# Performance work log

Measured on AMD Instinct MI355X. Metric: run time of the kernel, lower is better.

The kernel has to match this reference:

```python
import jax, jax.numpy as jnp
import numpy as np

N_NODES = 100000
N_EDGES = 1600000
D_IN = 64
D_HID = 64
D_ACT = 16


def gcn_conv(x, W, b, src, dst, n_nodes):
    """PyG-style GCNConv: D^-1/2 (A+I) D^-1/2 (x @ W) + b."""
    h = x @ W  # [N, out]
    ones = jnp.ones(src.shape[0], dtype=x.dtype)
    # degree with self-loops (in-degree + 1)
    deg = jax.ops.segment_sum(ones, dst, num_segments=n_nodes) + 1.0
    dinv = jax.lax.rsqrt(deg)  # [N]
    coef = dinv[src] * dinv[dst]  # [E]
    agg = jax.ops.segment_sum(h[src] * coef[:, None], dst, num_segments=n_nodes)
    agg = agg + h * (dinv * dinv)[:, None]  # self-loop term
    return agg + b


def setup_inputs() -> dict:
    key = jax.random.key(0)
    ks = jax.random.split(key, 6)
    x = jax.random.normal(ks[0], (N_NODES, D_IN), dtype=jnp.float32)
    edge_index = jax.random.randint(ks[1], (2, N_EDGES), 0, N_NODES, dtype=jnp.int64)
    s1 = 1.0 / np.sqrt(D_IN)
    s2 = 1.0 / np.sqrt(D_HID)
    W1 = jax.random.normal(ks[2], (D_IN, D_HID), dtype=jnp.float32) * s1
    b1 = jnp.zeros((D_HID,), dtype=jnp.float32)
    W2 = jax.random.normal(ks[3], (D_HID, D_HID), dtype=jnp.float32) * s2
    b2 = jnp.zeros((D_HID,), dtype=jnp.float32)
    Wfc = jax.random.normal(ks[4], (D_HID, D_ACT), dtype=jnp.float32) * s2
    bfc = jnp.zeros((D_ACT,), dtype=jnp.float32)
    return {"x": x, "edge_index": edge_index, "W1": W1, "b1": b1,
            "W2": W2, "b2": b2, "Wfc": Wfc, "bfc": bfc}


def reference(x, edge_index, W1, b1, W2, b2, Wfc, bfc):
    src, dst = edge_index[0], edge_index[1]
    n = x.shape[0]
    h = jax.nn.relu(gcn_conv(x, W1, b1, src, dst, n))
    h = jax.nn.relu(gcn_conv(h, W2, b2, src, dst, n))
    q_values = h @ Wfc + bfc
    return q_values
```

## Files before the change

### kernel.cpp

```cpp
#include <hip/hip_runtime.h>

#define NN 100000
#define NE 1600000
#define NCAP 64
#define NB2 782
#define NBP2 1024
#define CAP2 2560
#define CHUNK 2048
#define NCHUNK 782

typedef __attribute__((ext_vector_type(8))) short short8;
typedef __attribute__((ext_vector_type(4))) float f32x4;

static __device__ __forceinline__ unsigned short f2bf(float f) {
    unsigned u = __float_as_uint(f);
    u += 0x7fffu + ((u >> 16) & 1u);
    return (unsigned short)(u >> 16);
}
static __device__ __forceinline__ float bflo(unsigned u) { return __uint_as_float(u << 16); }
static __device__ __forceinline__ float bfhi(unsigned u) { return __uint_as_float(u & 0xffff0000u); }

static __device__ __forceinline__ short8 as_s8(uint4 u) {
    union { uint4 u4; short8 s8; } x; x.u4 = u; return x.s8;
}
static __device__ __forceinline__ f32x4 mfma16(short8 a, short8 b, f32x4 c) {
    return __builtin_amdgcn_mfma_f32_16x16x32_bf16(a, b, c, 0, 0, 0);
}

static __device__ __forceinline__ void split8(float4 a, float4 b, short8& hi8, short8& lo8) {
    float vv[8] = {a.x, a.y, a.z, a.w, b.x, b.y, b.z, b.w};
    unsigned h[8], l[8];
    #pragma unroll
    for (int j = 0; j < 8; ++j) {
        h[j] = f2bf(vv[j]);
        l[j] = f2bf(vv[j] - bflo(h[j]));
    }
    uint4 uh, ul;
    uh.x = h[0] | (h[1] << 16); uh.y = h[2] | (h[3] << 16);
    uh.z = h[4] | (h[5] << 16); uh.w = h[6] | (h[7] << 16);
    ul.x = l[0] | (l[1] << 16); ul.y = l[2] | (l[3] << 16);
    ul.z = l[4] | (l[5] << 16); ul.w = l[6] | (l[7] << 16);
    hi8 = as_s8(uh); lo8 = as_s8(ul);
}

__global__ __launch_bounds__(256) void bin_edges(const int* __restrict__ src,
                                                 const int* __restrict__ dst,
                                                 int* __restrict__ gcur,
                                                 int* __restrict__ pairs) {
    __shared__ int lcnt[NBP2];
    __shared__ int lnext[NBP2];
    int t = threadIdx.x;
    #pragma unroll
    for (int i = 0; i < 4; ++i) lcnt[t + 256 * i] = 0;
    __syncthreads();
    int base = blockIdx.x * CHUNK;
    int sr[8], dr[8];
    #pragma unroll
    for (int i = 0; i < 8; ++i) {
        int e = base + t + 256 * i;
        bool v = e < NE;
        sr[i] = v ? src[e] : 0;
        dr[i] = v ? dst[e] : -1;
        if (v) atomicAdd(&lcnt[dr[i] >> 7], 1);
    }
    __syncthreads();
    #pragma unroll
    for (int i = 0; i < 4; ++i) {
        int b = t + 256 * i;
        int v = lcnt[b];
        if (v) lnext[b] = b * CAP2 + atomicAdd(&gcur[b], v);
    }
    __syncthreads();
    #pragma unroll
    for (int i = 0; i < 8; ++i) {
        if (dr[i] >= 0) {
            int p = atomicAdd(&lnext[dr[i] >> 7], 1);
            pairs[p] = sr[i] | ((dr[i] & 127) << 17);
        }
    }
}

__global__ __launch_bounds__(256) void slab_place(const int* __restrict__ pairs,
                                                  const int* __restrict__ gcur,
                                                  int* __restrict__ esrc,
                                                  int* __restrict__ cnt,
                                                  float* __restrict__ dinv) {
    __shared__ int lc[128];
    int b = blockIdx.x;
    int t = threadIdx.x;
    if (t < 128) lc[t] = 0;
    __syncthreads();
    int e0 = b * CAP2;
    int e1 = e0 + min(gcur[b], CAP2);
    for (int i = e0 + t; i < e1; i += 256) {
        int w = pairs[i];
        int li = w >> 17;
        int p = atomicAdd(&lc[li], 1);
        if (p < NCAP - 1) esrc[(((b << 7) + li) << 6) + p] = w & 0x1FFFF;
    }
    __syncthreads();
    if (t < 128) {
        int node = (b << 7) + t;
        if (node < NN) {
            int c = lc[t];
            int cc = min(c, NCAP - 1);
            esrc[(node << 6) + cc] = node;
            cnt[node] = cc + 1;
            dinv[node] = rsqrtf((float)c + 1.0f);
        }
    }
}

__global__ void wpack(const float* __restrict__ W1, const float* __restrict__ W2,
                      uint4* __restrict__ P, int* __restrict__ gcur) {
    int tid = blockIdx.x * blockDim.x + threadIdx.x;
    if (tid >= 1024) return;
    gcur[tid] = 0;
    int w = tid >> 9;
    int f = tid & 511;
    int c = f >> 7;
    int t = (f >> 6) & 1;
    int lane = f & 63;
    const float* W = w ? W2 : W1;
    int k0 = t * 32 + (lane >> 4) * 8;
    int n  = c * 16 + (lane & 15);
    unsigned sh[8], sl[8];
    #pragma unroll
    for (int j = 0; j < 8; ++j) {
        float v = W[(k0 + j) * 64 + n];
        sh[j] = f2bf(v);
        sl[j] = f2bf(v - bflo(sh[j]));
    }
    uint4 ph, pl;
    ph.x = sh[0] | (sh[1] << 16); ph.y = sh[2] | (sh[3] << 16);
    ph.z = sh[4] | (sh[5] << 16); ph.w = sh[6] | (sh[7] << 16);
    pl.x = sl[0] | (sl[1] << 16); pl.y = sl[2] | (sl[3] << 16);
    pl.z = sl[4] | (sl[5] << 16); pl.w = sl[6] | (sl[7] << 16);
    P[w * 1024 + f]       = ph;
    P[w * 1024 + 512 + f] = pl;
}

__global__ __launch_bounds__(256) void gemm1_mfma(const float* __restrict__ X,
                                                  const uint4* __restrict__ WP,
                                                  const float* __restrict__ dinv,
                                                  uint4* __restrict__ G4) {
    __shared__ __align__(16) unsigned short Ls[4][16][64];
    int wave = threadIdx.x >> 6, lane = threadIdx.x & 63;
    int tile = blockIdx.x * 4 + wave;
    bool active = tile < (NN / 16);
    int node0 = (active ? tile : 0) * 16;
    int r = lane & 15, g = lane >> 4;

    const float* xr = X + (size_t)(node0 + r) * 64 + g * 8;
    float4 x0a = *(const float4*)(xr);
    float4 x0b = *(const float4*)(xr + 4);
    float4 x1a = *(const float4*)(xr + 32);
    float4 x1b = *(const float4*)(xr + 36);
    short8 ah0, al0, ah1, al1;
    split8(x0a, x0b, ah0, al0);
    split8(x1a, x1b, ah1, al1);

    f32x4 acc[4];
    #pragma unroll
    for (int c = 0; c < 4; ++c) acc[c] = (f32x4){0.f, 0.f, 0.f, 0.f};
    #pragma unroll
    for (int c = 0; c < 4; ++c) {
        short8 bh0 = as_s8(WP[(c * 2 + 0) * 64 + lane]);
        short8 bl0 = as_s8(WP[512 + (c * 2 + 0) * 64 + lane]);
        short8 bh1 = as_s8(WP[(c * 2 + 1) * 64 + lane]);
        short8 bl1 = as_s8(WP[512 + (c * 2 + 1) * 64 + lane]);
        acc[c] = mfma16(ah0, bh0, acc[c]);
        acc[c] = mfma16(al0, bh0, acc[c]);
        acc[c] = mfma16(ah0, bl0, acc[c]);
        acc[c] = mfma16(ah1, bh1, acc[c]);
        acc[c] = mfma16(al1, bh1, acc[c]);
        acc[c] = mfma16(ah1, bl1, acc[c]);
    }
    float dd[4];
    #pragma unroll
    for (int rr = 0; rr < 4; ++rr) dd[rr] = dinv[node0 + g * 4 + rr];
    #pragma unroll
    for (int c = 0; c < 4; ++c) {
        #pragma unroll
        for (int rr = 0; rr < 4; ++rr)
            Ls[wave][g * 4 + rr][c * 16 + r] = f2bf(acc[c][rr] * dd[rr]);
    }
    __syncthreads();
    if (active) {
        #pragma unroll
        for (int i = 0; i < 2; ++i) {
            int idx = lane + i * 64;
            int row = idx >> 3, u = idx & 7;
            G4[(size_t)(node0 + row) * 8 + u] = *(const uint4*)&Ls[wave][row][u * 8];
        }
    }
}

__global__ __launch_bounds__(256) void gemm2_mfma(const uint4* __restrict__ X4,
                                                  const uint4* __restrict__ WP,
                                                  const float* __restrict__ dinv,
                                                  uint4* __restrict__ G4) {
    __shared__ __align__(16) unsigned short Ls[4][16][64];
    int wave = threadIdx.x >> 6, lane = threadIdx.x & 63;
    int tile = blockIdx.x * 4 + wave;
    bool active = tile < (NN / 16);
    int node0 = (active ? tile : 0) * 16;
    int r = lane & 15, g = lane >> 4;

    short8 a0 = as_s8(X4[(size_t)(node0 + r) * 8 + g]);
    short8 a1 = as_s8(X4[(size_t)(node0 + r) * 8 + 4 + g]);

    f32x4 acc[4];
    #pragma unroll
    for (int c = 0; c < 4; ++c) acc[c] = (f32x4){0.f, 0.f, 0.f, 0.f};
    #pragma unroll
    for (int c = 0; c < 4; ++c) {
        short8 bh0 = as_s8(WP[(c * 2 + 0) * 64 + lane]);
        short8 bl0 = as_s8(WP[512 + (c * 2 + 0) * 64 + lane]);
        short8 bh1 = as_s8(WP[(c * 2 + 1) * 64 + lane]);
        short8 bl1 = as_s8(WP[512 + (c * 2 + 1) * 64 + lane]);
        acc[c] = mfma16(a0, bh0, acc[c]);
        acc[c] = mfma16(a0, bl0, acc[c]);
        acc[c] = mfma16(a1, bh1, acc[c]);
        acc[c] = mfma16(a1, bl1, acc[c]);
    }
    float dd[4];
    #pragma unroll
    for (int rr = 0; rr < 4; ++rr) dd[rr] = dinv[node0 + g * 4 + rr];
    #pragma unroll
    for (int c = 0; c < 4; ++c) {
        #pragma unroll
        for (int rr = 0; rr < 4; ++rr)
            Ls[wave][g * 4 + rr][c * 16 + r] = f2bf(acc[c][rr] * dd[rr]);
    }
    __syncthreads();
    if (active) {
        #pragma unroll
        for (int i = 0; i < 2; ++i) {
            int idx = lane + i * 64;
            int row = idx >> 3, u = idx & 7;
            G4[(size_t)(node0 + row) * 8 + u] = *(const uint4*)&Ls[wave][row][u * 8];
        }
    }
}

#define ACC8(u) do { \
    a0 += bflo((u).x); a1 += bfhi((u).x); a2 += bflo((u).y); a3 += bfhi((u).y); \
    a4 += bflo((u).z); a5 += bfhi((u).z); a6 += bflo((u).w); a7 += bfhi((u).w); } while (0)

#define GATHER_CORE(node)                                                     \
    int deg = cnt[node];                                                      \
    int sidx = esrc[((node) << 6) + (lane & 31)];                             \
    int nt = (deg - e + 7) >> 3;        \
    int s0 = __shfl(sidx, e);                                                 \
    int s1 = __shfl(sidx, e + 8);                                             \
    int s2 = __shfl(sidx, e + 16);                                            \
    int s3 = __shfl(sidx, e + 24);                                            \
    float a0 = 0.f, a1 = 0.f, a2 = 0.f, a3 = 0.f,                             \
          a4 = 0.f, a5 = 0.f, a6 = 0.f, a7 = 0.f;                             \
    uint4 u0, u1, u2, u3;                                                     \
    if (nt > 0) u0 = G4[s0 * 8 + m];                                          \
    if (nt > 1) u1 = G4[s1 * 8 + m];                                          \
    if (nt > 2) u2 = G4[s2 * 8 + m];                                          \
    if (nt > 3) u3 = G4[s3 * 8 + m];                                          \
    if (nt > 0) ACC8(u0);                                                     \
    if (nt > 1) ACC8(u1);                                                     \
    if (nt > 2) ACC8(u2);                                                     \
    if (nt > 3) ACC8(u3);                                                     \
    if (__any(nt > 4)) {                          \
        int shi = esrc[((node) << 6) + 32 + (lane & 31)];                     \
        int s4 = __shfl(shi, e);                                              \
        int s5 = __shfl(shi, e + 8);                                          \
        int s6 = __shfl(shi, e + 16);                                         \
        int s7 = __shfl(shi, e + 24);                                         \
        uint4 u4, u5, u6, u7;                                                 \
        if (nt > 4) u4 = G4[s4 * 8 + m];                                      \
        if (nt > 5) u5 = G4[s5 * 8 + m];                                      \
        if (nt > 6) u6 = G4[s6 * 8 + m];                                      \
        if (nt > 7) u7 = G4[s7 * 8 + m];                                      \
        if (nt > 4) ACC8(u4);                                                 \
        if (nt > 5) ACC8(u5);                                                 \
        if (nt > 6) ACC8(u6);                                                 \
        if (nt > 7) ACC8(u7);                                                 \
    }                                                                         \
    a0 += __shfl_xor(a0, 8);  a1 += __shfl_xor(a1, 8);                        \
    a2 += __shfl_xor(a2, 8);  a3 += __shfl_xor(a3, 8);                        \
    a4 += __shfl_xor(a4, 8);  a5 += __shfl_xor(a5, 8);                        \
    a6 += __shfl_xor(a6, 8);  a7 += __shfl_xor(a7, 8);                        \
    a0 += __shfl_xor(a0, 16); a1 += __shfl_xor(a1, 16);                       \
    a2 += __shfl_xor(a2, 16); a3 += __shfl_xor(a3, 16);                       \
    a4 += __shfl_xor(a4, 16); a5 += __shfl_xor(a5, 16);                       \
    a6 += __shfl_xor(a6, 16); a7 += __shfl_xor(a7, 16);                       \
    a0 += __shfl_xor(a0, 32); a1 += __shfl_xor(a1, 32);                       \
    a2 += __shfl_xor(a2, 32); a3 += __shfl_xor(a3, 32);                       \
    a4 += __shfl_xor(a4, 32); a5 += __shfl_xor(a5, 32);                       \
    a6 += __shfl_xor(a6, 32); a7 += __shfl_xor(a7, 32);

__global__ __launch_bounds__(256) void gather_bf16(
        const int* __restrict__ cnt, const int* __restrict__ esrc,
        const float* __restrict__ dinv, const uint4* __restrict__ G4,
        const float* __restrict__ b, uint4* __restrict__ outH) {
    int node = blockIdx.x * 4 + (threadIdx.x >> 6);
    int lane = threadIdx.x & 63;
    int e = lane >> 3, m = lane & 7;
    GATHER_CORE(node)
    if (e == 0) {
        float dd = dinv[node];
        float4 b0 = ((const float4*)b)[2 * m];
        float4 b1v = ((const float4*)b)[2 * m + 1];
        float h0 = fmaxf(fmaf(a0, dd, b0.x), 0.f);
        float h1 = fmaxf(fmaf(a1, dd, b0.y), 0.f);
        float h2 = fmaxf(fmaf(a2, dd, b0.z), 0.f);
        float h3 = fmaxf(fmaf(a3, dd, b0.w), 0.f);
        float h4 = fmaxf(fmaf(a4, dd, b1v.x), 0.f);
        float h5 = fmaxf(fmaf(a5, dd, b1v.y), 0.f);
        float h6 = fmaxf(fmaf(a6, dd, b1v.z), 0.f);
        float h7 = fmaxf(fmaf(a7, dd, b1v.w), 0.f);
        uint4 pk;
        pk.x = (unsigned)f2bf(h0) | ((unsigned)f2bf(h1) << 16);
        pk.y = (unsigned)f2bf(h2) | ((unsigned)f2bf(h3) << 16);
        pk.z = (unsigned)f2bf(h4) | ((unsigned)f2bf(h5) << 16);
        pk.w = (unsigned)f2bf(h6) | ((unsigned)f2bf(h7) << 16);
        outH[(size_t)node * 8 + m] = pk;
    }
}

__global__ __launch_bounds__(256) void gather_fc(
        const int* __restrict__ cnt, const int* __restrict__ esrc,
        const float* __restrict__ dinv, const uint4* __restrict__ G4,
        const float* __restrict__ b2, const float* __restrict__ Wfc,
        const float* __restrict__ bfc, float* __restrict__ out) {
    int node = blockIdx.x * 4 + (threadIdx.x >> 6);
    int lane = threadIdx.x & 63;
    int e = lane >> 3, m = lane & 7;
    int q = lane >> 4, c = lane & 15;
    float Wreg[16];
    #pragma unroll
    for (int i = 0; i < 16; ++i) Wreg[i] = Wfc[(q * 16 + i) * 16 + c];
    GATHER_CORE(node)
    float dd = dinv[node];
    float4 b0 = ((const float4*)b2)[2 * m];
    float4 b1v = ((const float4*)b2)[2 * m + 1];
    a0 = fmaxf(fmaf(a0, dd, b0.x), 0.f);
    a1 = fmaxf(fmaf(a1, dd, b0.y), 0.f);
    a2 = fmaxf(fmaf(a2, dd, b0.z), 0.f);
    a3 = fmaxf(fmaf(a3, dd, b0.w), 0.f);
    a4 = fmaxf(fmaf(a4, dd, b1v.x), 0.f);
    a5 = fmaxf(fmaf(a5, dd, b1v.y), 0.f);
    a6 = fmaxf(fmaf(a6, dd, b1v.z), 0.f);
    a7 = fmaxf(fmaf(a7, dd, b1v.w), 0.f);
    int sl0 = 2 * q, sl1 = 2 * q + 1;
    float acc = 0.f;
    acc = fmaf(__shfl(a0, sl0), Wreg[0], acc);
    acc = fmaf(__shfl(a1, sl0), Wreg[1], acc);
    acc = fmaf(__shfl(a2, sl0), Wreg[2], acc);
    acc = fmaf(__shfl(a3, sl0), Wreg[3], acc);
    acc = fmaf(__shfl(a4, sl0), Wreg[4], acc);
    acc = fmaf(__shfl(a5, sl0), Wreg[5], acc);
    acc = fmaf(__shfl(a6, sl0), Wreg[6], acc);
    acc = fmaf(__shfl(a7, sl0), Wreg[7], acc);
    acc = fmaf(__shfl(a0, sl1), Wreg[8], acc);
    acc = fmaf(__shfl(a1, sl1), Wreg[9], acc);
    acc = fmaf(__shfl(a2, sl1), Wreg[10], acc);
    acc = fmaf(__shfl(a3, sl1), Wreg[11], acc);
    acc = fmaf(__shfl(a4, sl1), Wreg[12], acc);
    acc = fmaf(__shfl(a5, sl1), Wreg[13], acc);
    acc = fmaf(__shfl(a6, sl1), Wreg[14], acc);
    acc = fmaf(__shfl(a7, sl1), Wreg[15], acc);
    acc += __shfl_xor(acc, 16);
    acc += __shfl_xor(acc, 32);
    if (lane < 16) out[node * 16 + c] = acc + bfc[c];
}

extern "C" void kernel_launch(void* const* d_in, const int* in_sizes, int n_in,
                              void* d_out, int out_size, void* d_ws, size_t ws_size,
                              hipStream_t stream) {
    const float* x   = (const float*)d_in[0];
    const int*   ei  = (const int*)d_in[1];
    const float* W1  = (const float*)d_in[2];
    const float* b1  = (const float*)d_in[3];
    const float* W2  = (const float*)d_in[4];
    const float* b2  = (const float*)d_in[5];
    const float* Wfc = (const float*)d_in[6];
    const float* bfc = (const float*)d_in[7];
    float* out = (float*)d_out;

    const int* src = ei;
    const int* dst = ei + NE;

    int*      gcur  = (int*)d_ws;
    int*      cnt   = gcur + NBP2;
    float*    dinvp = (float*)(cnt + NN);
    int*      esrc  = (int*)(dinvp + NN);
    unsigned* G     = (unsigned*)(esrc + (size_t)NN * NCAP);
    uint4*    bufB  = (uint4*)(G + (size_t)NN * 32);
    uint4*    WPK   = (uint4*)((unsigned*)bufB + (size_t)NN * 32);
    int*      pairs = (int*)bufB;

    wpack<<<4, 256, 0, stream>>>(W1, W2, WPK, gcur);
    bin_edges<<<NCHUNK, 256, 0, stream>>>(src, dst, gcur, pairs);
    slab_place<<<NB2, 256, 0, stream>>>(pairs, gcur, esrc, cnt, dinvp);

    gemm1_mfma<<<(NN / 16 + 3) / 4, 256, 0, stream>>>(x, WPK, dinvp, (uint4*)G);
    gather_bf16<<<NN / 4, 256, 0, stream>>>(cnt, esrc, dinvp, (const uint4*)G, b1, bufB);

    gemm2_mfma<<<(NN / 16 + 3) / 4, 256, 0, stream>>>(bufB, WPK + 1024, dinvp, (uint4*)G);
    gather_fc<<<NN / 4, 256, 0, stream>>>(cnt, esrc, dinvp, (const uint4*)G, b2, Wfc, bfc, out);
}
```

Baseline: 239.7 us.

## Shard edge-bin counters into eight groups and loop gather over edge slots

Edge binning now spreads each destination bin's global atomic counter and pair region across eight sub-slabs, chosen by block index. This reduces contention on the global atomicAdd, and slab_place walks all eight sub-slabs per bin. The gather core drops the fixed shuffle-based unrolled 8-edge scheme and uses a strided loop, two edges per iteration, that reads source indices directly from esrc. Per-group capacity is 384, so a skewed group could overflow and silently drop edges. The looped gather may also expose less memory-level parallelism than the old fully unrolled loads.

Measured after the change: 228.5 us. -4.6%, faster.

```diff
diff --git a/kernel.cpp b/kernel.cpp
--- a/kernel.cpp
+++ b/kernel.cpp
@@ -5,7 +5,7 @@
 #define NCAP 64
 #define NB2 782
 #define NBP2 1024
-#define CAP2 2560
+#define CAPG 384
 #define CHUNK 2048
 #define NCHUNK 782
 
@@ -50,6 +50,7 @@
     __shared__ int lcnt[NBP2];
     __shared__ int lnext[NBP2];
     int t = threadIdx.x;
+    int grp = blockIdx.x & 7;
     #pragma unroll
     for (int i = 0; i < 4; ++i) lcnt[t + 256 * i] = 0;
     __syncthreads();
@@ -68,7 +69,7 @@
     for (int i = 0; i < 4; ++i) {
         int b = t + 256 * i;
         int v = lcnt[b];
-        if (v) lnext[b] = b * CAP2 + atomicAdd(&gcur[b], v);
+        if (v) lnext[b] = ((grp << 10) + b) * CAPG + atomicAdd(&gcur[(grp << 10) + b], v);
     }
     __syncthreads();
     #pragma unroll
@@ -90,13 +91,17 @@
     int t = threadIdx.x;
     if (t < 128) lc[t] = 0;
     __syncthreads();
-    int e0 = b * CAP2;
-    int e1 = e0 + min(gcur[b], CAP2);
-    for (int i = e0 + t; i < e1; i += 256) {
-        int w = pairs[i];
-        int li = w >> 17;
-        int p = atomicAdd(&lc[li], 1);
-        if (p < NCAP - 1) esrc[(((b << 7) + li) << 6) + p] = w & 0x1FFFF;
+    #pragma unroll
+    for (int g = 0; g < 8; ++g) {
+        int rid = (g << 10) + b;
+        int e0 = rid * CAPG;
+        int n = min(gcur[rid], CAPG);
+        for (int i = t; i < n; i += 256) {
+            int w = pairs[e0 + i];
+            int li = w >> 17;
+            int p = atomicAdd(&lc[li], 1);
+            if (p < NCAP - 1) esrc[(((b << 7) + li) << 6) + p] = w & 0x1FFFF;
+        }
     }
     __syncthreads();
     if (t < 128) {
@@ -115,7 +120,8 @@
                       uint4* __restrict__ P, int* __restrict__ gcur) {
     int tid = blockIdx.x * blockDim.x + threadIdx.x;
     if (tid >= 1024) return;
-    gcur[tid] = 0;
+    #pragma unroll
+    for (int k = 0; k < 8; ++k) gcur[tid + 1024 * k] = 0;
     int w = tid >> 9;
     int f = tid & 511;
     int c = f >> 7;
@@ -246,42 +252,23 @@
 
 #define ACC8(u) do { \
     a0 += bflo((u).x); a1 += bfhi((u).x); a2 += bflo((u).y); a3 += bfhi((u).y); \
-    a4 += bflo((u).z); a5 += bfhi((u).z); a6 += bflo((u).w); a7 += bfhi((u).w); } while (0)
+    a4 += bflo((u).z); a5 += bfhi((u).z); a6 += bflo((u).w); a7 += bfhi(u.w); } while (0)
 
 #define GATHER_CORE(node)                                                     \
-    int deg = cnt[node];                                                      \
-    int sidx = esrc[((node) << 6) + (lane & 31)];                             \
-    int nt = (deg - e + 7) >> 3;        \
-    int s0 = __shfl(sidx, e);                                                 \
-    int s1 = __shfl(sidx, e + 8);                                             \
-    int s2 = __shfl(sidx, e + 16);                                            \
-    int s3 = __shfl(sidx, e + 24);                                            \
+    int j0 = (node) << 6;                                                     \
+    int e1 = j0 + cnt[node];                                                  \
     float a0 = 0.f, a1 = 0.f, a2 = 0.f, a3 = 0.f,                             \
           a4 = 0.f, a5 = 0.f, a6 = 0.f, a7 = 0.f;                             \
-    uint4 u0, u1, u2, u3;                                                     \
-    if (nt > 0) u0 = G4[s0 * 8 + m];                                          \
-    if (nt > 1) u1 = G4[s1 * 8 + m];                                          \
-    if (nt > 2) u2 = G4[s2 * 8 + m];                                          \
-    if (nt > 3) u3 = G4[s3 * 8 + m];                                          \
-    if (nt > 0) ACC8(u0);                                                     \
-    if (nt > 1) ACC8(u1);                                                     \
-    if (nt > 2) ACC8(u2);                                                     \
-    if (nt > 3) ACC8(u3);                                                     \
-    if (__any(nt > 4)) {                          \
-        int shi = esrc[((node) << 6) + 32 + (lane & 31)];                     \
-        int s4 = __shfl(shi, e);                                              \
-        int s5 = __shfl(shi, e + 8);                                          \
-        int s6 = __shfl(shi, e + 16);                                         \
-        int s7 = __shfl(shi, e + 24);                                         \
-        uint4 u4, u5, u6, u7;                                                 \
-        if (nt > 4) u4 = G4[s4 * 8 + m];                                      \
-        if (nt > 5) u5 = G4[s5 * 8 + m];                                      \
-        if (nt > 6) u6 = G4[s6 * 8 + m];                                      \
-        if (nt > 7) u7 = G4[s7 * 8 + m];                                      \
-        if (nt > 4) ACC8(u4);                                                 \
-        if (nt > 5) ACC8(u5);                                                 \
-        if (nt > 6) ACC8(u6);                                                 \
-        if (nt > 7) ACC8(u7);                                                 \
+    int j = j0 + e;                                                           \
+    for (; j + 8 < e1; j += 16) {                                             \
+        int s0 = esrc[j], s1 = esrc[j + 8];                                   \
+        uint4 u0 = G4[s0 * 8 + m];                                            \
+        uint4 u1 = G4[s1 * 8 + m];                                            \
+        ACC8(u0); ACC8(u1);                                                   \
+    }                                                                         \
+    for (; j < e1; j += 8) {                                                  \
+        uint4 u = G4[esrc[j] * 8 + m];                                        \
+        ACC8(u);                                                              \
     }                                                                         \
     a0 += __shfl_xor(a0, 8);  a1 += __shfl_xor(a1, 8);                        \
     a2 += __shfl_xor(a2, 8);  a3 += __shfl_xor(a3, 8);                        \
@@ -389,7 +376,7 @@
     const int* dst = ei + NE;
 
     int*      gcur  = (int*)d_ws;
-    int*      cnt   = gcur + NBP2;
+    int*      cnt   = gcur + 8192;
     float*    dinvp = (float*)(cnt + NN);
     int*      esrc  = (int*)(dinvp + NN);
     unsigned* G     = (unsigned*)(esrc + (size_t)NN * NCAP);
```
